# Kernel tuning notes

Hardware: AMD Instinct MI355X
Metric: run time of the kernel (lower is better)

The kernel has to match this reference:

```python
import jax, jax.numpy as jnp
import numpy as np

N_NODES = 100000
N_EDGES = 3200000
F_IN = 512
HIDDEN = 16
N_CLASSES = 16


def setup_inputs() -> dict:
    key = jax.random.key(0)
    k1, k2, k3, k4 = jax.random.split(key, 4)
    x = jax.random.normal(k1, (N_NODES, F_IN), dtype=jnp.float32)
    edge_index = jax.random.randint(k2, (2, N_EDGES), 0, N_NODES, dtype=jnp.int32)
    # Glorot-style init for GCN weights
    W1 = jax.random.normal(k3, (F_IN, HIDDEN), dtype=jnp.float32) * np.float32(np.sqrt(2.0 / (F_IN + HIDDEN)))
    b1 = jnp.zeros((HIDDEN,), dtype=jnp.float32)
    W2 = jax.random.normal(k4, (HIDDEN, N_CLASSES), dtype=jnp.float32) * np.float32(np.sqrt(2.0 / (HIDDEN + N_CLASSES)))
    b2 = jnp.zeros((N_CLASSES,), dtype=jnp.float32)
    return {"x": x, "W1": W1, "b1": b1, "W2": W2, "b2": b2, "edge_index": edge_index}


def _gcn_conv(x, src, dst, W, b, n_nodes):
    """PyG GCNConv: h = x @ W, then symmetric-normalized aggregation with self-loops, + bias."""
    h = x @ W  # [N, out]
    # degrees include self-loops (edge weight 1.0 everywhere)
    ones = jnp.ones(src.shape[0], dtype=h.dtype)
    deg = jax.ops.segment_sum(ones, dst, num_segments=n_nodes) + 1.0  # +1 for self-loop
    dinv = jax.lax.rsqrt(deg)  # deg >= 1, no zero guard needed
    norm = dinv[src] * dinv[dst]  # [E]
    agg = jax.ops.segment_sum(h[src] * norm[:, None], dst, num_segments=n_nodes)
    # self-loop contribution: norm_ii = 1/deg_i
    agg = agg + h * (dinv * dinv)[:, None]
    return agg + b


def reference(x, W1, b1, W2, b2, edge_index):
    src, dst = edge_index[0], edge_index[1]
    n = x.shape[0]
    h = jax.nn.relu(_gcn_conv(x, src, dst, W1, b1, n))
    # dropout is identity in eval mode
    out = _gcn_conv(h, src, dst, W2, b2, n)
    return jax.nn.log_softmax(out, axis=1)
```

## Files before the change

### kernel.cpp

```cpp
#include <hip/hip_runtime.h>
#include <hip/hip_bf16.h>
#include <math.h>

constexpr int N_NODES = 100000;
constexpr int N_EDGES = 3200000;
constexpr int F_IN    = 512;
constexpr int HID     = 16;

constexpr int NPAD = 100352;

constexpr int B_BITS = 8;
constexpr int NPB    = 1 << B_BITS;
constexpr int NBKT   = (N_NODES + NPB - 1) / NPB;
constexpr int SBLK   = 400;
constexpr int CHUNK  = N_EDGES / SBLK;
constexpr int CAP    = 10240;

typedef float f32x4 __attribute__((ext_vector_type(4)));
typedef short bfrag8 __attribute__((ext_vector_type(8)));

__device__ __forceinline__ unsigned short f2bf_rne(float f) {
    unsigned int u = __float_as_uint(f);
    u += 0x7FFFu + ((u >> 16) & 1u);
    return (unsigned short)(u >> 16);
}
__device__ __forceinline__ float bf2f(unsigned short u) {
    return __uint_as_float((unsigned int)u << 16);
}

__global__ __launch_bounds__(256) void prep_kernel(const float* __restrict__ W1,
                                                   unsigned short* __restrict__ w1t,
                                                   int* __restrict__ gcur,
                                                   unsigned short* __restrict__ hh_bf,
                                                   unsigned short* __restrict__ hh2_bf) {
    int i = blockIdx.x * 256 + threadIdx.x;
    if (i < F_IN * HID) {
        int k = i >> 4, n = i & 15;
        w1t[n * F_IN + k] = f2bf_rne(W1[i]);
    }
    if (i < NBKT) gcur[i] = i * CAP;
    if (i < 16) {
        hh_bf [N_NODES * 16 + i] = 0;
        hh2_bf[N_NODES * 16 + i] = 0;
    }
}

__global__ __launch_bounds__(1024) void bin_scatter_kernel(const int* __restrict__ src,
                                                           const int* __restrict__ dst,
                                                           int* __restrict__ gcur,
                                                           unsigned int* __restrict__ binned) {
    __shared__ int sdst[CHUNK];
    __shared__ int ssrc[CHUNK];
    __shared__ int cnt[NBKT];
    __shared__ int cur[NBKT];
    const int tid = threadIdx.x;
    for (int t = tid; t < NBKT; t += 1024) cnt[t] = 0;
    const int base = blockIdx.x * CHUNK;
    for (int i = tid; i < CHUNK; i += 1024) {
        sdst[i] = dst[base + i];
        ssrc[i] = src[base + i];
    }
    __syncthreads();
    for (int i = tid; i < CHUNK; i += 1024)
        atomicAdd(&cnt[sdst[i] >> B_BITS], 1);
    __syncthreads();
    for (int t = tid; t < NBKT; t += 1024)
        cur[t] = cnt[t] ? atomicAdd(&gcur[t], cnt[t]) : 0;
    __syncthreads();
    for (int i = tid; i < CHUNK; i += 1024) {
        int d = sdst[i];
        int b = d >> B_BITS;
        int pos = atomicAdd(&cur[b], 1);
        binned[pos] = ((unsigned)(d & (NPB - 1)) << 24) | (unsigned)ssrc[i];
    }
}

__global__ __launch_bounds__(1024) void csr_bucket_kernel(const unsigned int* __restrict__ binned,
                                                          const int* __restrict__ gcur,
                                                          int2* __restrict__ row2,
                                                          int* __restrict__ csr,
                                                          float* __restrict__ dinv,
                                                          int* __restrict__ perm) {
    __shared__ unsigned int eb[CAP];
    __shared__ int deg[NPB];
    __shared__ int pre[NPB];
    __shared__ int cur[NPB];
    __shared__ int hist[64];
    __shared__ int hoff[64];
    __shared__ int hcur[64];
    const int tid = threadIdx.x;
    const int b = blockIdx.x;
    const int e0 = b * CAP;
    int ne = gcur[b] - e0;
    if (ne > CAP) ne = CAP;
    if (ne < 0) ne = 0;

    if (tid < NPB) deg[tid] = 0;
    if (tid < 64) hist[tid] = 0;
    for (int i = tid; i < ne; i += 1024) eb[i] = binned[e0 + i];
    __syncthreads();
    for (int i = tid; i < ne; i += 1024)
        atomicAdd(&deg[eb[i] >> 24], 1);
    __syncthreads();
    int pd = 0;
    if (tid < NPB) {
        pd = (deg[tid] + 3) & ~3;
        pre[tid] = pd;
        atomicAdd(&hist[min(pd >> 2, 63)], 1);
    }
    __syncthreads();
    for (int off = 1; off < NPB; off <<= 1) {
        int v = 0;
        if (tid < NPB && tid >= off) v = pre[tid - off];
        __syncthreads();
        if (tid < NPB) pre[tid] += v;
        __syncthreads();
    }
    if (tid < 64) hoff[tid] = hist[tid];
    __syncthreads();
    for (int off = 1; off < 64; off <<= 1) {
        int v = 0;
        if (tid < 64 && tid >= off) v = hoff[tid - off];
        __syncthreads();
        if (tid < 64) hoff[tid] += v;
        __syncthreads();
    }
    if (tid < 64) hcur[tid] = (tid == 0) ? 0 : hoff[tid - 1];
    __syncthreads();
    if (tid < NPB) {
        int excl = (tid == 0) ? 0 : pre[tid - 1];
        int start = e0 + excl;
        cur[tid] = start;
        int node = b * NPB + tid;
        if (node < N_NODES) {
            row2[node] = make_int2(start, start + pd);
            dinv[node] = rsqrtf((float)deg[tid] + 1.0f);
        }
        int rank = atomicAdd(&hcur[min(pd >> 2, 63)], 1);
        perm[b * NPB + rank] = node;
    }
    __syncthreads();
    for (int i = tid; i < ne; i += 1024) {
        unsigned int v = eb[i];
        int pos = atomicAdd(&cur[v >> 24], 1);
        csr[pos] = (int)(v & 0xFFFFFFu);
    }
    if (tid < NPB) {
        int node = b * NPB + tid;
        if (node < N_NODES) {
            int d = deg[tid];
            int pdl = (d + 3) & ~3;
            int s = e0 + ((tid == 0) ? 0 : pre[tid - 1]) + d;
            for (int q = d; q < pdl; ++q) csr[s++] = N_NODES;
        }
    }
}

__global__ __launch_bounds__(256) void gemm1_kernel(const float* __restrict__ x,
                                                    const unsigned short* __restrict__ w1t,
                                                    const float* __restrict__ b1,
                                                    const float* __restrict__ dinv,
                                                    unsigned short* __restrict__ hh_bf,
                                                    float* __restrict__ aggs1) {
    const int tid  = threadIdx.x;
    const int lane = tid & 63;
    const int wv   = tid >> 6;
    const int m    = lane & 15;
    const int quad = lane >> 4;
    const int node0 = blockIdx.x * 64 + wv * 16;

    int gm = node0 + m; if (gm >= N_NODES) gm = N_NODES - 1;
    const float* arow = x + (size_t)gm * F_IN + quad * 8;

    bfrag8 bfr[16];
    const unsigned short* wbase = w1t + m * F_IN + quad * 8;
    #pragma unroll
    for (int t = 0; t < 16; ++t)
        bfr[t] = *(const bfrag8*)(wbase + t * 32);

    f32x4 acc = {0.f, 0.f, 0.f, 0.f};
    #pragma unroll 4
    for (int t = 0; t < 16; ++t) {
        float4 lo = *(const float4*)(arow + t * 32);
        float4 hi = *(const float4*)(arow + t * 32 + 4);
        union { bfrag8 fr; __hip_bfloat162 h2[4]; } u;
        u.h2[0] = __float22bfloat162_rn(float2{lo.x, lo.y});
        u.h2[1] = __float22bfloat162_rn(float2{lo.z, lo.w});
        u.h2[2] = __float22bfloat162_rn(float2{hi.x, hi.y});
        u.h2[3] = __float22bfloat162_rn(float2{hi.z, hi.w});
        acc = __builtin_amdgcn_mfma_f32_16x16x32_bf16(u.fr, bfr[t], acc, 0, 0, 0);
    }

    const float b1j = b1[m];
    #pragma unroll
    for (int r = 0; r < 4; ++r) {
        int gn = node0 + quad * 4 + r;
        if (gn < N_NODES) {
            float dv = dinv[gn];
            float hv = acc[r] * dv;
            size_t o = (size_t)gn * 16 + m;
            hh_bf[o] = f2bf_rne(hv);
            aggs1[o] = hv * dv + b1j;
        }
    }
}

__global__ __launch_bounds__(256) void pull1_kernel(const unsigned short* __restrict__ hh_bf,
                                                    const float* __restrict__ aggs1,
                                                    const float* __restrict__ dinv,
                                                    const int2* __restrict__ row2,
                                                    const int* __restrict__ csr,
                                                    const int* __restrict__ perm,
                                                    const float* __restrict__ W2,
                                                    const float* __restrict__ b2,
                                                    unsigned short* __restrict__ hh2_bf,
                                                    float* __restrict__ aggs2) {
    __shared__ f32x4 w2s[64];
    __shared__ f32x4 b2s[4];
    const int tid = threadIdx.x;
    if (tid < 64) w2s[tid] = ((const f32x4*)W2)[tid];
    if (tid < 4)  b2s[tid] = ((const f32x4*)b2)[tid];
    __syncthreads();

    int t = blockIdx.x * 256 + tid;
    int node = perm[t >> 2];
    int l = t & 3;
    if (node >= N_NODES) return;

    int2 re = row2[node];
    int p = re.x, e = re.y;
    const unsigned short* hb = hh_bf + (l << 2);
    f32x4 a0 = {0,0,0,0}, a1 = {0,0,0,0}, a2 = {0,0,0,0}, a3 = {0,0,0,0};
    for (; p < e; p += 4) {
        int4 s = *(const int4*)(csr + p);
        ushort4 g0 = *(const ushort4*)(hb + (s.x << 4));
        ushort4 g1 = *(const ushort4*)(hb + (s.y << 4));
        ushort4 g2 = *(const ushort4*)(hb + (s.z << 4));
        ushort4 g3 = *(const ushort4*)(hb + (s.w << 4));
        a0.x += bf2f(g0.x); a0.y += bf2f(g0.y); a0.z += bf2f(g0.z); a0.w += bf2f(g0.w);
        a1.x += bf2f(g1.x); a1.y += bf2f(g1.y); a1.z += bf2f(g1.z); a1.w += bf2f(g1.w);
        a2.x += bf2f(g2.x); a2.y += bf2f(g2.y); a2.z += bf2f(g2.z); a2.w += bf2f(g2.w);
        a3.x += bf2f(g3.x); a3.y += bf2f(g3.y); a3.z += bf2f(g3.z); a3.w += bf2f(g3.w);
    }
    f32x4 a = (a0 + a1) + (a2 + a3);
    float dv = dinv[node];
    f32x4 base = *(const f32x4*)(aggs1 + ((size_t)node << 4) + (l << 2));
    float v[4];
    #pragma unroll
    for (int c = 0; c < 4; ++c) v[c] = fmaxf(base[c] + dv * a[c], 0.f);

    f32x4 h2 = {0.f, 0.f, 0.f, 0.f};
    #pragma unroll
    for (int k = 0; k < 16; ++k) {
        float vk = __shfl(v[k & 3], k >> 2, 4);
        f32x4 w = w2s[k * 4 + l];
        h2.x += vk * w.x; h2.y += vk * w.y; h2.z += vk * w.z; h2.w += vk * w.w;
    }
    f32x4 bb = b2s[l];
    ushort4 hs;
    f32x4 ag;
    float hv0 = h2.x * dv; hs.x = f2bf_rne(hv0); ag.x = hv0 * dv + bb.x;
    float hv1 = h2.y * dv; hs.y = f2bf_rne(hv1); ag.y = hv1 * dv + bb.y;
    float hv2 = h2.z * dv; hs.z = f2bf_rne(hv2); ag.z = hv2 * dv + bb.z;
    float hv3 = h2.w * dv; hs.w = f2bf_rne(hv3); ag.w = hv3 * dv + bb.w;
    size_t o = ((size_t)node << 4) + (l << 2);
    *(ushort4*)(hh2_bf + o) = hs;
    *(f32x4*)(aggs2 + o) = ag;
}

__global__ __launch_bounds__(256) void pull2_kernel(const unsigned short* __restrict__ hh2_bf,
                                                    const float* __restrict__ aggs2,
                                                    const float* __restrict__ dinv,
                                                    const int2* __restrict__ row2,
                                                    const int* __restrict__ csr,
                                                    const int* __restrict__ perm,
                                                    float* __restrict__ out) {
    int t = blockIdx.x * 256 + threadIdx.x;
    int node = perm[t >> 2];
    int l = t & 3;
    if (node >= N_NODES) return;

    int2 re = row2[node];
    int p = re.x, e = re.y;
    const unsigned short* hb = hh2_bf + (l << 2);
    f32x4 a0 = {0,0,0,0}, a1 = {0,0,0,0}, a2 = {0,0,0,0}, a3 = {0,0,0,0};
    for (; p < e; p += 4) {
        int4 s = *(const int4*)(csr + p);
        ushort4 g0 = *(const ushort4*)(hb + (s.x << 4));
        ushort4 g1 = *(const ushort4*)(hb + (s.y << 4));
        ushort4 g2 = *(const ushort4*)(hb + (s.z << 4));
        ushort4 g3 = *(const ushort4*)(hb + (s.w << 4));
        a0.x += bf2f(g0.x); a0.y += bf2f(g0.y); a0.z += bf2f(g0.z); a0.w += bf2f(g0.w);
        a1.x += bf2f(g1.x); a1.y += bf2f(g1.y); a1.z += bf2f(g1.z); a1.w += bf2f(g1.w);
        a2.x += bf2f(g2.x); a2.y += bf2f(g2.y); a2.z += bf2f(g2.z); a2.w += bf2f(g2.w);
        a3.x += bf2f(g3.x); a3.y += bf2f(g3.y); a3.z += bf2f(g3.z); a3.w += bf2f(g3.w);
    }
    f32x4 a = (a0 + a1) + (a2 + a3);
    float dv = dinv[node];
    f32x4 base = *(const f32x4*)(aggs2 + ((size_t)node << 4) + (l << 2));
    f32x4 o4;
    o4.x = base.x + dv * a.x; o4.y = base.y + dv * a.y;
    o4.z = base.z + dv * a.z; o4.w = base.w + dv * a.w;

    float m = fmaxf(fmaxf(o4.x, o4.y), fmaxf(o4.z, o4.w));
    m = fmaxf(m, __shfl_xor(m, 1));
    m = fmaxf(m, __shfl_xor(m, 2));
    float s = expf(o4.x - m) + expf(o4.y - m) + expf(o4.z - m) + expf(o4.w - m);
    s += __shfl_xor(s, 1);
    s += __shfl_xor(s, 2);
    float ls = m + logf(s);
    f32x4 r;
    r.x = o4.x - ls; r.y = o4.y - ls; r.z = o4.z - ls; r.w = o4.w - ls;
    *(f32x4*)(out + ((size_t)node << 4) + (l << 2)) = r;
}

extern "C" void kernel_launch(void* const* d_in, const int* in_sizes, int n_in,
                              void* d_out, int out_size, void* d_ws, size_t ws_size,
                              hipStream_t stream) {
    const float* x    = (const float*)d_in[0];
    const float* W1   = (const float*)d_in[1];
    const float* b1   = (const float*)d_in[2];
    const float* W2   = (const float*)d_in[3];
    const float* b2   = (const float*)d_in[4];
    const int*   ei   = (const int*)d_in[5];
    const int*   src  = ei;
    const int*   dst  = ei + N_EDGES;
    float* out = (float*)d_out;

    constexpr size_t SLOTS    = (size_t)NBKT * CAP;
    constexpr size_t OFF_DINV = 512;
    constexpr size_t OFF_ROW2 = 512 + (size_t)NPAD;
    constexpr size_t OFF_PERM = 512 + 3 * (size_t)NPAD;
    constexpr size_t OFF_CSR  = 512 + 4 * (size_t)NPAD;
    constexpr size_t OFF_HH   = OFF_CSR + SLOTS;
    constexpr size_t OFF_AG1  = OFF_HH + 800512;
    constexpr size_t OFF_HH2  = OFF_AG1 + 1600000;
    constexpr size_t OFF_AG2  = OFF_HH2 + 800512;
    constexpr size_t OFF_W1T  = OFF_AG2 + 1600000;

    int*   wsi  = (int*)d_ws;
    float* wsf  = (float*)d_ws;
    int*   gcur  = wsi;
    float* dinv  = wsf + OFF_DINV;
    int2*  row2  = (int2*)(wsi + OFF_ROW2);
    int*   perm  = wsi + OFF_PERM;
    int*   csr   = wsi + OFF_CSR;
    unsigned int* binned = (unsigned int*)csr;
    unsigned short* hh_bf  = (unsigned short*)(wsi + OFF_HH);
    float*          aggs1  = wsf + OFF_AG1;
    unsigned short* hh2_bf = (unsigned short*)(wsi + OFF_HH2);
    float*          aggs2  = wsf + OFF_AG2;
    unsigned short* w1t    = (unsigned short*)(wsi + OFF_W1T);

    const int MB  = (N_NODES + 63) / 64;
    const int GB4 = (NBKT * NPB * 4) / 256;

    prep_kernel       <<<32, 256, 0, stream>>>(W1, w1t, gcur, hh_bf, hh2_bf);
    bin_scatter_kernel<<<SBLK, 1024, 0, stream>>>(src, dst, gcur, binned);
    csr_bucket_kernel <<<NBKT, 1024, 0, stream>>>(binned, gcur, row2, csr, dinv, perm);
    gemm1_kernel      <<<MB, 256, 0, stream>>>(x, w1t, b1, dinv, hh_bf, aggs1);
    pull1_kernel      <<<GB4, 256, 0, stream>>>(hh_bf, aggs1, dinv, row2, csr, perm, W2, b2, hh2_bf, aggs2);
    pull2_kernel      <<<GB4, 256, 0, stream>>>(hh2_bf, aggs2, dinv, row2, csr, perm, out);
}
```

Before: 451.2 us.

## Drop degree-sorted node permutation and unroll gather loop by eight

```diff
diff --git a/kernel.cpp b/kernel.cpp
--- a/kernel.cpp
+++ b/kernel.cpp
@@ -79,15 +79,11 @@
                                                           const int* __restrict__ gcur,
                                                           int2* __restrict__ row2,
                                                           int* __restrict__ csr,
-                                                          float* __restrict__ dinv,
-                                                          int* __restrict__ perm) {
+                                                          float* __restrict__ dinv) {
     __shared__ unsigned int eb[CAP];
     __shared__ int deg[NPB];
     __shared__ int pre[NPB];
     __shared__ int cur[NPB];
-    __shared__ int hist[64];
-    __shared__ int hoff[64];
-    __shared__ int hcur[64];
     const int tid = threadIdx.x;
     const int b = blockIdx.x;
     const int e0 = b * CAP;
@@ -96,18 +92,12 @@
     if (ne < 0) ne = 0;
 
     if (tid < NPB) deg[tid] = 0;
-    if (tid < 64) hist[tid] = 0;
     for (int i = tid; i < ne; i += 1024) eb[i] = binned[e0 + i];
     __syncthreads();
     for (int i = tid; i < ne; i += 1024)
         atomicAdd(&deg[eb[i] >> 24], 1);
     __syncthreads();
-    int pd = 0;
-    if (tid < NPB) {
-        pd = (deg[tid] + 3) & ~3;
-        pre[tid] = pd;
-        atomicAdd(&hist[min(pd >> 2, 63)], 1);
-    }
+    if (tid < NPB) pre[tid] = (deg[tid] + 3) & ~3;
     __syncthreads();
     for (int off = 1; off < NPB; off <<= 1) {
         int v = 0;
@@ -116,28 +106,16 @@
         if (tid < NPB) pre[tid] += v;
         __syncthreads();
     }
-    if (tid < 64) hoff[tid] = hist[tid];
-    __syncthreads();
-    for (int off = 1; off < 64; off <<= 1) {
-        int v = 0;
-        if (tid < 64 && tid >= off) v = hoff[tid - off];
-        __syncthreads();
-        if (tid < 64) hoff[tid] += v;
-        __syncthreads();
-    }
-    if (tid < 64) hcur[tid] = (tid == 0) ? 0 : hoff[tid - 1];
-    __syncthreads();
     if (tid < NPB) {
         int excl = (tid == 0) ? 0 : pre[tid - 1];
         int start = e0 + excl;
         cur[tid] = start;
         int node = b * NPB + tid;
         if (node < N_NODES) {
+            int pd = (deg[tid] + 3) & ~3;
             row2[node] = make_int2(start, start + pd);
             dinv[node] = rsqrtf((float)deg[tid] + 1.0f);
         }
-        int rank = atomicAdd(&hcur[min(pd >> 2, 63)], 1);
-        perm[b * NPB + rank] = node;
     }
     __syncthreads();
     for (int i = tid; i < ne; i += 1024) {
@@ -210,7 +188,6 @@
                                                     const float* __restrict__ dinv,
                                                     const int2* __restrict__ row2,
                                                     const int* __restrict__ csr,
-                                                    const int* __restrict__ perm,
                                                     const float* __restrict__ W2,
                                                     const float* __restrict__ b2,
                                                     unsigned short* __restrict__ hh2_bf,
@@ -223,7 +200,7 @@
     __syncthreads();
 
     int t = blockIdx.x * 256 + tid;
-    int node = perm[t >> 2];
+    int node = t >> 2;
     int l = t & 3;
     if (node >= N_NODES) return;
 
@@ -231,7 +208,28 @@
     int p = re.x, e = re.y;
     const unsigned short* hb = hh_bf + (l << 2);
     f32x4 a0 = {0,0,0,0}, a1 = {0,0,0,0}, a2 = {0,0,0,0}, a3 = {0,0,0,0};
-    for (; p < e; p += 4) {
+    f32x4 a4 = {0,0,0,0}, a5 = {0,0,0,0}, a6 = {0,0,0,0}, a7 = {0,0,0,0};
+    for (; p + 8 <= e; p += 8) {
+        int4 sA = *(const int4*)(csr + p);
+        int4 sB = *(const int4*)(csr + p + 4);
+        ushort4 g0 = *(const ushort4*)(hb + (sA.x << 4));
+        ushort4 g1 = *(const ushort4*)(hb + (sA.y << 4));
+        ushort4 g2 = *(const ushort4*)(hb + (sA.z << 4));
+        ushort4 g3 = *(const ushort4*)(hb + (sA.w << 4));
+        ushort4 g4 = *(const ushort4*)(hb + (sB.x << 4));
+        ushort4 g5 = *(const ushort4*)(hb + (sB.y << 4));
+        ushort4 g6 = *(const ushort4*)(hb + (sB.z << 4));
+        ushort4 g7 = *(const ushort4*)(hb + (sB.w << 4));
+        a0.x += bf2f(g0.x); a0.y += bf2f(g0.y); a0.z += bf2f(g0.z); a0.w += bf2f(g0.w);
+        a1.x += bf2f(g1.x); a1.y += bf2f(g1.y); a1.z += bf2f(g1.z); a1.w += bf2f(g1.w);
+        a2.x += bf2f(g2.x); a2.y += bf2f(g2.y); a2.z += bf2f(g2.z); a2.w += bf2f(g2.w);
+        a3.x += bf2f(g3.x); a3.y += bf2f(g3.y); a3.z += bf2f(g3.z); a3.w += bf2f(g3.w);
+        a4.x += bf2f(g4.x); a4.y += bf2f(g4.y); a4.z += bf2f(g4.z); a4.w += bf2f(g4.w);
+        a5.x += bf2f(g5.x); a5.y += bf2f(g5.y); a5.z += bf2f(g5.z); a5.w += bf2f(g5.w);
+        a6.x += bf2f(g6.x); a6.y += bf2f(g6.y); a6.z += bf2f(g6.z); a6.w += bf2f(g6.w);
+        a7.x += bf2f(g7.x); a7.y += bf2f(g7.y); a7.z += bf2f(g7.z); a7.w += bf2f(g7.w);
+    }
+    if (p < e) {
         int4 s = *(const int4*)(csr + p);
         ushort4 g0 = *(const ushort4*)(hb + (s.x << 4));
         ushort4 g1 = *(const ushort4*)(hb + (s.y << 4));
@@ -242,7 +240,7 @@
         a2.x += bf2f(g2.x); a2.y += bf2f(g2.y); a2.z += bf2f(g2.z); a2.w += bf2f(g2.w);
         a3.x += bf2f(g3.x); a3.y += bf2f(g3.y); a3.z += bf2f(g3.z); a3.w += bf2f(g3.w);
     }
-    f32x4 a = (a0 + a1) + (a2 + a3);
+    f32x4 a = ((a0 + a1) + (a2 + a3)) + ((a4 + a5) + (a6 + a7));
     float dv = dinv[node];
     f32x4 base = *(const f32x4*)(aggs1 + ((size_t)node << 4) + (l << 2));
     float v[4];
@@ -273,10 +271,9 @@
                                                     const float* __restrict__ dinv,
                                                     const int2* __restrict__ row2,
                                                     const int* __restrict__ csr,
-                                                    const int* __restrict__ perm,
                                                     float* __restrict__ out) {
     int t = blockIdx.x * 256 + threadIdx.x;
-    int node = perm[t >> 2];
+    int node = t >> 2;
     int l = t & 3;
     if (node >= N_NODES) return;
 
@@ -284,7 +281,28 @@
     int p = re.x, e = re.y;
     const unsigned short* hb = hh2_bf + (l << 2);
     f32x4 a0 = {0,0,0,0}, a1 = {0,0,0,0}, a2 = {0,0,0,0}, a3 = {0,0,0,0};
-    for (; p < e; p += 4) {
+    f32x4 a4 = {0,0,0,0}, a5 = {0,0,0,0}, a6 = {0,0,0,0}, a7 = {0,0,0,0};
+    for (; p + 8 <= e; p += 8) {
+        int4 sA = *(const int4*)(csr + p);
+        int4 sB = *(const int4*)(csr + p + 4);
+        ushort4 g0 = *(const ushort4*)(hb + (sA.x << 4));
+        ushort4 g1 = *(const ushort4*)(hb + (sA.y << 4));
+        ushort4 g2 = *(const ushort4*)(hb + (sA.z << 4));
+        ushort4 g3 = *(const ushort4*)(hb + (sA.w << 4));
+        ushort4 g4 = *(const ushort4*)(hb + (sB.x << 4));
+        ushort4 g5 = *(const ushort4*)(hb + (sB.y << 4));
+        ushort4 g6 = *(const ushort4*)(hb + (sB.z << 4));
+        ushort4 g7 = *(const ushort4*)(hb + (sB.w << 4));
+        a0.x += bf2f(g0.x); a0.y += bf2f(g0.y); a0.z += bf2f(g0.z); a0.w += bf2f(g0.w);
+        a1.x += bf2f(g1.x); a1.y += bf2f(g1.y); a1.z += bf2f(g1.z); a1.w += bf2f(g1.w);
+        a2.x += bf2f(g2.x); a2.y += bf2f(g2.y); a2.z += bf2f(g2.z); a2.w += bf2f(g2.w);
+        a3.x += bf2f(g3.x); a3.y += bf2f(g3.y); a3.z += bf2f(g3.z); a3.w += bf2f(g3.w);
+        a4.x += bf2f(g4.x); a4.y += bf2f(g4.y); a4.z += bf2f(g4.z); a4.w += bf2f(g4.w);
+        a5.x += bf2f(g5.x); a5.y += bf2f(g5.y); a5.z += bf2f(g5.z); a5.w += bf2f(g5.w);
+        a6.x += bf2f(g6.x); a6.y += bf2f(g6.y); a6.z += bf2f(g6.z); a6.w += bf2f(g6.w);
+        a7.x += bf2f(g7.x); a7.y += bf2f(g7.y); a7.z += bf2f(g7.z); a7.w += bf2f(g7.w);
+    }
+    if (p < e) {
         int4 s = *(const int4*)(csr + p);
         ushort4 g0 = *(const ushort4*)(hb + (s.x << 4));
         ushort4 g1 = *(const ushort4*)(hb + (s.y << 4));
@@ -295,7 +313,7 @@
         a2.x += bf2f(g2.x); a2.y += bf2f(g2.y); a2.z += bf2f(g2.z); a2.w += bf2f(g2.w);
         a3.x += bf2f(g3.x); a3.y += bf2f(g3.y); a3.z += bf2f(g3.z); a3.w += bf2f(g3.w);
     }
-    f32x4 a = (a0 + a1) + (a2 + a3);
+    f32x4 a = ((a0 + a1) + (a2 + a3)) + ((a4 + a5) + (a6 + a7));
     float dv = dinv[node];
     f32x4 base = *(const f32x4*)(aggs2 + ((size_t)node << 4) + (l << 2));
     f32x4 o4;
@@ -330,8 +348,7 @@
     constexpr size_t SLOTS    = (size_t)NBKT * CAP;
     constexpr size_t OFF_DINV = 512;
     constexpr size_t OFF_ROW2 = 512 + (size_t)NPAD;
-    constexpr size_t OFF_PERM = 512 + 3 * (size_t)NPAD;
-    constexpr size_t OFF_CSR  = 512 + 4 * (size_t)NPAD;
+    constexpr size_t OFF_CSR  = 512 + 3 * (size_t)NPAD;
     constexpr size_t OFF_HH   = OFF_CSR + SLOTS;
     constexpr size_t OFF_AG1  = OFF_HH + 800512;
     constexpr size_t OFF_HH2  = OFF_AG1 + 1600000;
@@ -343,7 +360,6 @@
     int*   gcur  = wsi;
     float* dinv  = wsf + OFF_DINV;
     int2*  row2  = (int2*)(wsi + OFF_ROW2);
-    int*   perm  = wsi + OFF_PERM;
     int*   csr   = wsi + OFF_CSR;
     unsigned int* binned = (unsigned int*)csr;
     unsigned short* hh_bf  = (unsigned short*)(wsi + OFF_HH);
@@ -353,12 +369,12 @@
     unsigned short* w1t    = (unsigned short*)(wsi + OFF_W1T);
 
     const int MB  = (N_NODES + 63) / 64;
-    const int GB4 = (NBKT * NPB * 4) / 256;
+    const int GB4 = (N_NODES * 4 + 255) / 256;
 
     prep_kernel       <<<32, 256, 0, stream>>>(W1, w1t, gcur, hh_bf, hh2_bf);
     bin_scatter_kernel<<<SBLK, 1024, 0, stream>>>(src, dst, gcur, binned);
-    csr_bucket_kernel <<<NBKT, 1024, 0, stream>>>(binned, gcur, row2, csr, dinv, perm);
+    csr_bucket_kernel <<<NBKT, 1024, 0, stream>>>(binned, gcur, row2, csr, dinv);
     gemm1_kernel      <<<MB, 256, 0, stream>>>(x, w1t, b1, dinv, hh_bf, aggs1);
-    pull1_kernel      <<<GB4, 256, 0, stream>>>(hh_bf, aggs1, dinv, row2, csr, perm, W2, b2, hh2_bf, aggs2);
-    pull2_kernel      <<<GB4, 256, 0, stream>>>(hh2_bf, aggs2, dinv, row2, csr, perm, out);
-}
+    pull1_kernel      <<<GB4, 256, 0, stream>>>(hh_bf, aggs1, dinv, row2, csr, W2, b2, hh2_bf, aggs2);
+    pull2_kernel      <<<GB4, 256, 0, stream>>>(hh2_bf, aggs2, dinv, row2, csr, out);
+}
```

Result: faster. 437.8 us (-3.0%).
